# Kernel optimization log

Measured on AMD Instinct MI355X. Metric: run time of the kernel, lower is better.

The kernel has to match this reference:

```python
import jax, jax.numpy as jnp
import numpy as np

NUM_GRAPHS = 256
NUM_LAYERS = 4
HIDDEN = 256
N_FEATS = 9
VOCAB = 119
BN_EPS = 1e-5


def setup_inputs() -> dict:
    key = jax.random.key(0)
    ks = jax.random.split(key, 16)
    N, E, H = 10000, 320000, HIDDEN
    x = jax.random.randint(ks[0], (N, N_FEATS), 0, 2, dtype=jnp.int64)
    edge_index = jax.random.randint(ks[1], (2, E), 0, N, dtype=jnp.int64)
    batch_ids = jnp.sort(jax.random.randint(ks[2], (N,), 0, NUM_GRAPHS, dtype=jnp.int64))
    s = 1.0 / np.sqrt(H)
    emb = jax.random.normal(ks[3], (N_FEATS, VOCAB, H), jnp.float32) * 0.02
    W = jax.random.normal(ks[4], (NUM_LAYERS, H, H), jnp.float32) * s
    b = jnp.zeros((NUM_LAYERS, H), jnp.float32)
    gamma = jnp.ones((NUM_LAYERS, H), jnp.float32)
    beta = jnp.zeros((NUM_LAYERS, H), jnp.float32)
    mlp_W1 = jax.random.normal(ks[5], (H, H // 2), jnp.float32) * s
    mlp_b1 = jnp.zeros((H // 2,), jnp.float32)
    mlp_W2 = jax.random.normal(ks[6], (H // 2, H // 4), jnp.float32) * (1.0 / np.sqrt(H // 2))
    mlp_b2 = jnp.zeros((H // 4,), jnp.float32)
    mlp_W3 = jax.random.normal(ks[7], (H // 4, 1), jnp.float32) * (1.0 / np.sqrt(H // 4))
    mlp_b3 = jnp.zeros((1,), jnp.float32)
    return dict(x=x, edge_index=edge_index, batch_ids=batch_ids, emb=emb, W=W, b=b,
                gamma=gamma, beta=beta, mlp_W1=mlp_W1, mlp_b1=mlp_b1,
                mlp_W2=mlp_W2, mlp_b2=mlp_b2, mlp_W3=mlp_W3, mlp_b3=mlp_b3)


def reference(x, edge_index, batch_ids, emb, W, b, gamma, beta,
              mlp_W1, mlp_b1, mlp_W2, mlp_b2, mlp_W3, mlp_b3):
    N = x.shape[0]
    src, dst = edge_index[0], edge_index[1]

    # AtomEncoder: sum of per-feature embeddings. emb[f, x[:,f]] -> [N, 9, H]
    h = jnp.sum(emb[jnp.arange(N_FEATS), x], axis=1)

    # GCN normalization with self-loops: deg_i = 1 + in-degree, norm = deg^-1/2
    deg = 1.0 + jax.ops.segment_sum(jnp.ones_like(dst, jnp.float32), dst, num_segments=N)
    nrm = jax.lax.rsqrt(deg)
    edge_w = (nrm[src] * nrm[dst])[:, None]   # [E,1]
    self_w = (nrm * nrm)[:, None]             # [N,1]

    for l in range(NUM_LAYERS):
        identity = h
        hw = h @ W[l]                                     # dense GEMM [N,H]x[H,H]
        agg = jax.ops.segment_sum(hw[src] * edge_w, dst, num_segments=N) + hw * self_w
        h = agg + b[l]
        # BatchNorm1d (training statistics over nodes)
        mu = jnp.mean(h, axis=0)
        var = jnp.var(h, axis=0)
        h = (h - mu) * jax.lax.rsqrt(var + BN_EPS) * gamma[l] + beta[l]
        h = jax.nn.relu(h)
        h = h + identity  # residual

    # global mean pool over graph ids
    sums = jax.ops.segment_sum(h, batch_ids, num_segments=NUM_GRAPHS)
    cnt = jax.ops.segment_sum(jnp.ones((N,), jnp.float32), batch_ids, num_segments=NUM_GRAPHS)
    g = sums / jnp.maximum(cnt, 1.0)[:, None]             # [G, H]

    # MLP head [H, H/2, H/4, 1]
    g = jax.nn.relu(g @ mlp_W1 + mlp_b1)
    g = jax.nn.relu(g @ mlp_W2 + mlp_b2)
    return g @ mlp_W3 + mlp_b3
```

## Files before the change

### kernel.cpp

```cpp
#include <hip/hip_runtime.h>

#define HID 256
#define NFEAT 9
#define VOCAB 119
#define NLAYERS 4
#define NGRAPHS 256
#define BN_EPS 1e-5f

typedef short short8 __attribute__((ext_vector_type(8)));
typedef float floatx4 __attribute__((ext_vector_type(4)));

__device__ inline unsigned short f2bf(float f) {
    unsigned int u = __float_as_uint(f);
    unsigned int r = u + 0x7FFF + ((u >> 16) & 1);
    return (unsigned short)(r >> 16);
}
__device__ inline float bf2f(unsigned short u) {
    return __uint_as_float(((unsigned int)u) << 16);
}

__global__ __launch_bounds__(256) void setup_misc(
        const int* __restrict__ x, const float* __restrict__ emb,
        const float* __restrict__ W,
        int* __restrict__ degi, int* __restrict__ fillc, float* __restrict__ bnsums,
        unsigned short* __restrict__ wt, unsigned short* __restrict__ hbA,
        int N, int zb) {
    const int bx = blockIdx.x;
    const int tid = threadIdx.x;
    __shared__ float sw[32][33];
    __shared__ int xf[NFEAT];

    if (bx < zb) {
        int i = bx * 256 + tid;
        if (i < N) { degi[i] = 0; fillc[i] = 0; }
        if (bx == 0) {
            for (int j = tid; j < NLAYERS * 2 * HID; j += 256) bnsums[j] = 0.f;
        }
    } else if (bx < zb + 256) {
        int j = bx - zb;
        int l = j >> 6;
        int rem = j & 63;
        int k0 = (rem >> 3) * 32, n0 = (rem & 7) * 32;
        int c = tid & 31, r8 = tid >> 5;
        const float* Wl = W + (size_t)l * HID * HID;
        unsigned short* Wtl = wt + (size_t)l * HID * HID;
#pragma unroll
        for (int p = 0; p < 4; ++p) {
            int r = r8 + p * 8;
            sw[r][c] = Wl[(k0 + r) * HID + n0 + c];
        }
        __syncthreads();
#pragma unroll
        for (int p = 0; p < 4; ++p) {
            int r = r8 + p * 8;
            Wtl[(size_t)(n0 + r) * HID + k0 + c] = f2bf(sw[c][r]);
        }
    } else {
        int n = bx - zb - 256;
        if (n < N) {
            if (tid < NFEAT) xf[tid] = x[n * NFEAT + tid];
            __syncthreads();
            float s = 0.f;
#pragma unroll
            for (int f = 0; f < NFEAT; ++f) s += emb[(size_t)(f * VOCAB + xf[f]) * HID + tid];
            hbA[(size_t)n * HID + tid] = f2bf(s);
        }
    }
}

__global__ void deg_kernel(const int* __restrict__ dst, int* __restrict__ degi, int E) {
    int i = blockIdx.x * blockDim.x + threadIdx.x;
    if (i < E) atomicAdd(&degi[dst[i]], 1);
}

__global__ __launch_bounds__(1024) void scan_kernel(const int* __restrict__ degi,
                                                    int* __restrict__ row_ptr,
                                                    float* __restrict__ nrm, int N) {
    int tid = threadIdx.x;
    int ch = (N + 1023) >> 10;
    int i0 = tid * ch;
    int i1 = min(i0 + ch, N);
    if (i0 > N) i0 = N;
    int local = 0;
    for (int i = i0; i < i1; ++i) local += degi[i];
    int lane = tid & 63, wid = tid >> 6;
    int v = local;
#pragma unroll
    for (int off = 1; off < 64; off <<= 1) {
        int u = __shfl_up(v, off);
        if (lane >= off) v += u;
    }
    __shared__ int wsum[16];
    if (lane == 63) wsum[wid] = v;
    __syncthreads();
    if (tid < 16) {
        int w = wsum[tid];
#pragma unroll
        for (int off = 1; off < 16; off <<= 1) {
            int u = __shfl_up(w, off);
            if (tid >= off) w += u;
        }
        wsum[tid] = w;
    }
    __syncthreads();
    int base = (wid > 0 ? wsum[wid - 1] : 0) + (v - local);
    int run = base;
    for (int i = i0; i < i1; ++i) {
        int d = degi[i];
        row_ptr[i] = run;
        run += d;
        nrm[i] = rsqrtf(1.0f + (float)d);
    }
    if (tid == 0) row_ptr[N] = wsum[15];
}

__global__ void fill_kernel(const int* __restrict__ src, const int* __restrict__ dst,
                            const int* __restrict__ row_ptr, int* __restrict__ fill,
                            const float* __restrict__ nrm,
                            int2* __restrict__ edges, int E) {
    int i = blockIdx.x * blockDim.x + threadIdx.x;
    if (i < E) {
        int d = dst[i];
        int s = src[i];
        int pos = row_ptr[d] + atomicAdd(&fill[d], 1);
        int2 rec;
        rec.x = s;
        rec.y = __float_as_int(nrm[s] * nrm[d]);
        edges[pos] = rec;
    }
}

__global__ __launch_bounds__(256) void agg_shfl_kernel(const unsigned short* __restrict__ hb,
                                                       const int* __restrict__ row_ptr,
                                                       const int2* __restrict__ edges,
                                                       const float* __restrict__ nrm,
                                                       unsigned short* __restrict__ aggb, int N) {
    int tid = threadIdx.x;
    int wave = tid >> 6;
    int lane = tid & 63;
    int sub = lane >> 5;
    int sl = lane & 31;
    int n = blockIdx.x * 4 + wave;
    if (n >= N) return;
    int co = sl * 8;
    int s = row_ptr[n], e = row_ptr[n + 1];
    int len = e - s;
    int h0 = (len + 1) >> 1;
    int base = s + sub * h0;
    int cnt = sub ? (len - h0) : h0;
    float a[8];
#pragma unroll
    for (int j = 0; j < 8; ++j) a[j] = 0.f;

    int done = 0;
    while (done < cnt) {
        int m = min(32, cnt - done);
        int li = done + (sl < m ? sl : m - 1);
        int2 rec = edges[base + li];
        int j = 0;
        for (; j + 1 < m; j += 2) {
            int s0 = __shfl(rec.x, j, 32);
            int s1 = __shfl(rec.x, j + 1, 32);
            float w0 = __int_as_float(__shfl(rec.y, j, 32));
            float w1 = __int_as_float(__shfl(rec.y, j + 1, 32));
            short8 u0 = *(const short8*)&hb[(size_t)s0 * HID + co];
            short8 u1 = *(const short8*)&hb[(size_t)s1 * HID + co];
#pragma unroll
            for (int k = 0; k < 8; ++k)
                a[k] += w0 * bf2f((unsigned short)u0[k]) + w1 * bf2f((unsigned short)u1[k]);
        }
        if (j < m) {
            int s0 = __shfl(rec.x, j, 32);
            float w0 = __int_as_float(__shfl(rec.y, j, 32));
            short8 u0 = *(const short8*)&hb[(size_t)s0 * HID + co];
#pragma unroll
            for (int k = 0; k < 8; ++k) a[k] += w0 * bf2f((unsigned short)u0[k]);
        }
        done += m;
    }
#pragma unroll
    for (int j = 0; j < 8; ++j) a[j] += __shfl_xor(a[j], 32);
    if (sub == 0) {
        float nd = nrm[n];
        float sw2 = nd * nd;
        short8 us = *(const short8*)&hb[(size_t)n * HID + co];
        short8 o;
#pragma unroll
        for (int j = 0; j < 8; ++j) {
            float v = a[j] + sw2 * bf2f((unsigned short)us[j]);
            o[j] = (short)f2bf(v);
        }
        *(short8*)&aggb[(size_t)n * HID + co] = o;
    }
}

__global__ __launch_bounds__(256) void mfma_gemm128(const unsigned short* __restrict__ A,
                                                    const unsigned short* __restrict__ Bt,
                                                    const float* __restrict__ bias,
                                                    unsigned short* __restrict__ C,
                                                    float* __restrict__ sums, int M) {
    __shared__ unsigned short As[128][40];
    __shared__ unsigned short Bs[64][40];
    __shared__ float lsum[64];
    __shared__ float lsq[64];
    int tid = threadIdx.x;
    int row0 = blockIdx.x * 128;
    int col0 = blockIdx.y * 64;
    int lane = tid & 63;
    int wid = tid >> 6;
    int arow = tid >> 1;
    int akc = (tid & 1) * 16;
    int brow = tid >> 2;
    int bkc = (tid & 3) * 8;
    int wm = (wid & 1) * 64;
    int wn = (wid >> 1) * 32;
    int quad = lane >> 4;
    int ln = lane & 15;

    floatx4 acc[4][2];
#pragma unroll
    for (int r = 0; r < 4; ++r)
#pragma unroll
        for (int c = 0; c < 2; ++c) acc[r][c] = (floatx4){0.f, 0.f, 0.f, 0.f};

    if (tid < 64) { lsum[tid] = 0.f; lsq[tid] = 0.f; }

    for (int kk = 0; kk < HID; kk += 32) {
        short8 av0 = {0, 0, 0, 0, 0, 0, 0, 0};
        short8 av1 = {0, 0, 0, 0, 0, 0, 0, 0};
        int ar = row0 + arow;
        if (ar < M) {
            av0 = *(const short8*)&A[(size_t)ar * HID + kk + akc];
            av1 = *(const short8*)&A[(size_t)ar * HID + kk + akc + 8];
        }
        short8 bv = *(const short8*)&Bt[(size_t)(col0 + brow) * HID + kk + bkc];
        *(short8*)&As[arow][akc] = av0;
        *(short8*)&As[arow][akc + 8] = av1;
        *(short8*)&Bs[brow][bkc] = bv;
        __syncthreads();
        short8 bf0 = *(const short8*)&Bs[wn + ln][quad * 8];
        short8 bf1 = *(const short8*)&Bs[wn + 16 + ln][quad * 8];
#pragma unroll
        for (int r = 0; r < 4; ++r) {
            short8 af = *(const short8*)&As[wm + r * 16 + ln][quad * 8];
            acc[r][0] = __builtin_amdgcn_mfma_f32_16x16x32_bf16(af, bf0, acc[r][0], 0, 0, 0);
            acc[r][1] = __builtin_amdgcn_mfma_f32_16x16x32_bf16(af, bf1, acc[r][1], 0, 0, 0);
        }
        __syncthreads();
    }
    float bias0 = bias[col0 + wn + ln];
    float bias1 = bias[col0 + wn + 16 + ln];
    float p0 = 0.f, q0 = 0.f, p1 = 0.f, q1 = 0.f;
#pragma unroll
    for (int r = 0; r < 4; ++r) {
#pragma unroll
        for (int rr = 0; rr < 4; ++rr) {
            int row = row0 + wm + r * 16 + quad * 4 + rr;
            if (row < M) {
                float v0 = acc[r][0][rr] + bias0;
                float v1 = acc[r][1][rr] + bias1;
                C[(size_t)row * HID + col0 + wn + ln] = f2bf(v0);
                C[(size_t)row * HID + col0 + wn + 16 + ln] = f2bf(v1);
                p0 += v0; q0 += v0 * v0;
                p1 += v1; q1 += v1 * v1;
            }
        }
    }
    atomicAdd(&lsum[wn + ln], p0);
    atomicAdd(&lsq[wn + ln], q0);
    atomicAdd(&lsum[wn + 16 + ln], p1);
    atomicAdd(&lsq[wn + 16 + ln], q1);
    __syncthreads();
    if (tid < 64) {
        unsafeAtomicAdd(&sums[col0 + tid], lsum[tid]);
        unsafeAtomicAdd(&sums[HID + col0 + tid], lsq[tid]);
    }
}

__global__ __launch_bounds__(256) void bn_kernel(const unsigned short* __restrict__ hwb,
                                                 const float* __restrict__ sums,
                                                 const float* __restrict__ gamma,
                                                 const float* __restrict__ beta,
                                                 const unsigned short* __restrict__ hold,
                                                 unsigned short* __restrict__ hbnew, int N) {
    int i4 = blockIdx.x * blockDim.x + threadIdx.x;
    int base = i4 * 4;
    if (base >= N * HID) return;
    int c = base & (HID - 1);
    float invN = 1.0f / (float)N;
    float4 s4 = *(const float4*)&sums[c];
    float4 q4 = *(const float4*)&sums[HID + c];
    float4 g4 = *(const float4*)&gamma[c];
    float4 be4 = *(const float4*)&beta[c];
    ushort4 v = *(const ushort4*)&hwb[base];
    ushort4 r = *(const ushort4*)&hold[base];
    ushort4 o;
    {
        float mu = s4.x * invN, var = q4.x * invN - mu * mu;
        o.x = f2bf(fmaxf((bf2f(v.x) - mu) * g4.x * rsqrtf(var + BN_EPS) + be4.x, 0.f) + bf2f(r.x));
        mu = s4.y * invN; var = q4.y * invN - mu * mu;
        o.y = f2bf(fmaxf((bf2f(v.y) - mu) * g4.y * rsqrtf(var + BN_EPS) + be4.y, 0.f) + bf2f(r.y));
        mu = s4.z * invN; var = q4.z * invN - mu * mu;
        o.z = f2bf(fmaxf((bf2f(v.z) - mu) * g4.z * rsqrtf(var + BN_EPS) + be4.z, 0.f) + bf2f(r.z));
        mu = s4.w * invN; var = q4.w * invN - mu * mu;
        o.w = f2bf(fmaxf((bf2f(v.w) - mu) * g4.w * rsqrtf(var + BN_EPS) + be4.w, 0.f) + bf2f(r.w));
    }
    *(ushort4*)&hbnew[base] = o;
}

__device__ inline int lower_bound_g(const int* __restrict__ a, int n, int key) {
    int lo = 0, hi = n;
    while (lo < hi) {
        int mid = (lo + hi) >> 1;
        if (a[mid] < key) lo = mid + 1; else hi = mid;
    }
    return lo;
}

__global__ __launch_bounds__(256) void pool_mlp_bn_kernel(
        const unsigned short* __restrict__ hwb,
        const float* __restrict__ sums,
        const float* __restrict__ gamma,
        const float* __restrict__ beta,
        const unsigned short* __restrict__ resid,
        const int* __restrict__ batch, int N,
        const float* __restrict__ W1, const float* __restrict__ b1,
        const float* __restrict__ W2, const float* __restrict__ b2,
        const float* __restrict__ W3, const float* __restrict__ b3,
        float* __restrict__ out) {
    int g = blockIdx.x, tid = threadIdx.x;
    int lo = lower_bound_g(batch, N, g);
    int hi = lower_bound_g(batch, N, g + 1);
    float invN = 1.0f / (float)N;
    float mu = sums[tid] * invN;
    float var = sums[HID + tid] * invN - mu * mu;
    float sc = gamma[tid] * rsqrtf(var + BN_EPS);
    float be = beta[tid];
    float s = 0.f;
    for (int i = lo; i < hi; ++i) {
        float v = (bf2f(hwb[(size_t)i * HID + tid]) - mu) * sc + be;
        v = fmaxf(v, 0.f) + bf2f(resid[(size_t)i * HID + tid]);
        s += v;
    }
    __shared__ float gs[256];
    __shared__ float t1[128];
    __shared__ float t2[64];
    float inv = 1.0f / fmaxf((float)(hi - lo), 1.0f);
    gs[tid] = s * inv;
    __syncthreads();
    if (tid < 128) {
        float a = b1[tid];
        for (int k = 0; k < 256; ++k) a += gs[k] * W1[k * 128 + tid];
        t1[tid] = fmaxf(a, 0.f);
    }
    __syncthreads();
    if (tid < 64) {
        float a = b2[tid];
        for (int k = 0; k < 128; ++k) a += t1[k] * W2[k * 64 + tid];
        t2[tid] = fmaxf(a, 0.f);
    }
    __syncthreads();
    if (tid < 64) {
        float p = t2[tid] * W3[tid];
#pragma unroll
        for (int off = 32; off >= 1; off >>= 1) p += __shfl_down(p, off);
        if (tid == 0) out[g] = p + b3[0];
    }
}

extern "C" void kernel_launch(void* const* d_in, const int* in_sizes, int n_in,
                              void* d_out, int out_size, void* d_ws, size_t ws_size,
                              hipStream_t stream) {
    const int* x      = (const int*)d_in[0];
    const int* ei     = (const int*)d_in[1];
    const int* batch  = (const int*)d_in[2];
    const float* emb  = (const float*)d_in[3];
    const float* W    = (const float*)d_in[4];
    const float* b    = (const float*)d_in[5];
    const float* gamma= (const float*)d_in[6];
    const float* beta = (const float*)d_in[7];
    const float* W1   = (const float*)d_in[8];
    const float* b1   = (const float*)d_in[9];
    const float* W2   = (const float*)d_in[10];
    const float* b2   = (const float*)d_in[11];
    const float* W3   = (const float*)d_in[12];
    const float* b3   = (const float*)d_in[13];
    float* out = (float*)d_out;

    int N = in_sizes[0] / NFEAT;
    int E = in_sizes[1] / 2;
    const int* srcp = ei;
    const int* dstp = ei + E;

    char* ws = (char*)d_ws;
    auto alloc = [&](size_t bytes) -> char* {
        char* p = ws;
        ws += (bytes + 255) & ~(size_t)255;
        return p;
    };
    int* degi     = (int*)alloc((size_t)N * 4);
    int* row_ptr  = (int*)alloc((size_t)(N + 1) * 4);
    int* fillc    = (int*)alloc((size_t)N * 4);
    float* nrm    = (float*)alloc((size_t)N * 4);
    int2* edges   = (int2*)alloc((size_t)E * 8);
    unsigned short* hbA  = (unsigned short*)alloc((size_t)N * HID * 2);
    unsigned short* hbB  = (unsigned short*)alloc((size_t)N * HID * 2);
    unsigned short* aggb = (unsigned short*)alloc((size_t)N * HID * 2);
    unsigned short* hwb  = (unsigned short*)alloc((size_t)N * HID * 2);
    unsigned short* wt   = (unsigned short*)alloc((size_t)NLAYERS * HID * HID * 2);
    float* bnsums = (float*)alloc((size_t)NLAYERS * 2 * HID * 4);

    int zb = (N + 255) / 256;
    int miscGrid = zb + 256 + N;
    setup_misc<<<miscGrid, 256, 0, stream>>>(x, emb, W, degi, fillc, bnsums, wt, hbA, N, zb);
    deg_kernel<<<(E + 255) / 256, 256, 0, stream>>>(dstp, degi, E);
    scan_kernel<<<1, 1024, 0, stream>>>(degi, row_ptr, nrm, N);
    fill_kernel<<<(E + 255) / 256, 256, 0, stream>>>(srcp, dstp, row_ptr, fillc, nrm, edges, E);

    unsigned short* hbcur = hbA;
    unsigned short* hboth = hbB;
    for (int l = 0; l < NLAYERS; ++l) {
        float* lsums = bnsums + (size_t)l * 2 * HID;
        agg_shfl_kernel<<<(N + 3) / 4, 256, 0, stream>>>(hbcur, row_ptr, edges, nrm, aggb, N);
        dim3 ggrid((N + 127) / 128, 4);
        mfma_gemm128<<<ggrid, 256, 0, stream>>>(aggb, wt + (size_t)l * HID * HID,
                                                b + (size_t)l * HID, hwb, lsums, N);
        if (l < NLAYERS - 1) {
            bn_kernel<<<((size_t)N * HID / 4 + 255) / 256, 256, 0, stream>>>(
                hwb, lsums, gamma + (size_t)l * HID, beta + (size_t)l * HID,
                hbcur, hboth, N);
            unsigned short* tb = hbcur; hbcur = hboth; hboth = tb;
        }
    }

    pool_mlp_bn_kernel<<<NGRAPHS, 256, 0, stream>>>(
        hwb, bnsums + (size_t)3 * 2 * HID, gamma + (size_t)3 * HID, beta + (size_t)3 * HID,
        hbcur, batch, N, W1, b1, W2, b2, W3, b3, out);
}
```

Baseline: 302.4 us.

## Split aggregation into column halves with four edge groups per wave

The aggregation kernel now launches twice as many blocks, each handling half of the 256 feature columns. Each wave is split into four 16-lane groups that process different edges at the same time, instead of two 32-lane halves covering all columns. This raises memory-level parallelism per wave and shortens the serial edge loop per node, which should help hide gather latency. In exchange, edge records are read twice (once per column half) and the reduction needs an extra cross-lane shuffle step.

```diff
diff --git a/kernel.cpp b/kernel.cpp
--- a/kernel.cpp
+++ b/kernel.cpp
@@ -130,65 +130,69 @@
     }
 }
 
-__global__ __launch_bounds__(256) void agg_shfl_kernel(const unsigned short* __restrict__ hb,
-                                                       const int* __restrict__ row_ptr,
-                                                       const int2* __restrict__ edges,
-                                                       const float* __restrict__ nrm,
-                                                       unsigned short* __restrict__ aggb, int N) {
+__global__ __launch_bounds__(256) void agg_g4_kernel(const unsigned short* __restrict__ hb,
+                                                     const int* __restrict__ row_ptr,
+                                                     const int2* __restrict__ edges,
+                                                     const float* __restrict__ nrm,
+                                                     unsigned short* __restrict__ aggb, int N) {
+    int bx = blockIdx.x;
+    int half = bx & 1;
     int tid = threadIdx.x;
     int wave = tid >> 6;
     int lane = tid & 63;
-    int sub = lane >> 5;
-    int sl = lane & 31;
-    int n = blockIdx.x * 4 + wave;
+    int g = lane >> 4;
+    int sl = lane & 15;
+    int n = (bx >> 1) * 4 + wave;
     if (n >= N) return;
-    int co = sl * 8;
+    int co = half * 128 + sl * 8;
+    const unsigned short* hbc = hb + co;
     int s = row_ptr[n], e = row_ptr[n + 1];
     int len = e - s;
-    int h0 = (len + 1) >> 1;
-    int base = s + sub * h0;
-    int cnt = sub ? (len - h0) : h0;
     float a[8];
 #pragma unroll
-    for (int j = 0; j < 8; ++j) a[j] = 0.f;
+    for (int k = 0; k < 8; ++k) a[k] = 0.f;
 
     int done = 0;
-    while (done < cnt) {
-        int m = min(32, cnt - done);
-        int li = done + (sl < m ? sl : m - 1);
-        int2 rec = edges[base + li];
+    while (done < len) {
+        int m = min(64, len - done);
+        int li = done + (lane < m ? lane : m - 1);
+        int2 rec = edges[s + li];
+        int mq = m & ~3;
         int j = 0;
-        for (; j + 1 < m; j += 2) {
-            int s0 = __shfl(rec.x, j, 32);
-            int s1 = __shfl(rec.x, j + 1, 32);
-            float w0 = __int_as_float(__shfl(rec.y, j, 32));
-            float w1 = __int_as_float(__shfl(rec.y, j + 1, 32));
-            short8 u0 = *(const short8*)&hb[(size_t)s0 * HID + co];
-            short8 u1 = *(const short8*)&hb[(size_t)s1 * HID + co];
-#pragma unroll
-            for (int k = 0; k < 8; ++k)
-                a[k] += w0 * bf2f((unsigned short)u0[k]) + w1 * bf2f((unsigned short)u1[k]);
+        for (; j < mq; j += 4) {
+            int jj = j + g;
+            int src = __shfl(rec.x, jj, 64);
+            float w = __int_as_float(__shfl(rec.y, jj, 64));
+            short8 u = *(const short8*)&hbc[(size_t)src * HID];
+#pragma unroll
+            for (int k = 0; k < 8; ++k) a[k] += w * bf2f((unsigned short)u[k]);
         }
         if (j < m) {
-            int s0 = __shfl(rec.x, j, 32);
-            float w0 = __int_as_float(__shfl(rec.y, j, 32));
-            short8 u0 = *(const short8*)&hb[(size_t)s0 * HID + co];
-#pragma unroll
-            for (int k = 0; k < 8; ++k) a[k] += w0 * bf2f((unsigned short)u0[k]);
+            int jj = j + g;
+            int cj = jj < m ? jj : (m - 1);
+            int src = __shfl(rec.x, cj, 64);
+            float w = __int_as_float(__shfl(rec.y, cj, 64));
+            if (jj >= m) w = 0.f;
+            short8 u = *(const short8*)&hbc[(size_t)src * HID];
+#pragma unroll
+            for (int k = 0; k < 8; ++k) a[k] += w * bf2f((unsigned short)u[k]);
         }
         done += m;
     }
 #pragma unroll
-    for (int j = 0; j < 8; ++j) a[j] += __shfl_xor(a[j], 32);
-    if (sub == 0) {
+    for (int k = 0; k < 8; ++k) {
+        a[k] += __shfl_xor(a[k], 16);
+        a[k] += __shfl_xor(a[k], 32);
+    }
+    if (g == 0) {
         float nd = nrm[n];
         float sw2 = nd * nd;
-        short8 us = *(const short8*)&hb[(size_t)n * HID + co];
+        short8 us = *(const short8*)&hbc[(size_t)n * HID];
         short8 o;
 #pragma unroll
-        for (int j = 0; j < 8; ++j) {
-            float v = a[j] + sw2 * bf2f((unsigned short)us[j]);
-            o[j] = (short)f2bf(v);
+        for (int k = 0; k < 8; ++k) {
+            float v = a[k] + sw2 * bf2f((unsigned short)us[k]);
+            o[k] = (short)f2bf(v);
         }
         *(short8*)&aggb[(size_t)n * HID + co] = o;
     }
@@ -419,9 +423,10 @@
 
     unsigned short* hbcur = hbA;
     unsigned short* hboth = hbB;
+    int aggGrid = ((N + 3) / 4) * 2;
     for (int l = 0; l < NLAYERS; ++l) {
         float* lsums = bnsums + (size_t)l * 2 * HID;
-        agg_shfl_kernel<<<(N + 3) / 4, 256, 0, stream>>>(hbcur, row_ptr, edges, nrm, aggb, N);
+        agg_g4_kernel<<<aggGrid, 256, 0, stream>>>(hbcur, row_ptr, edges, nrm, aggb, N);
         dim3 ggrid((N + 127) / 128, 4);
         mfma_gemm128<<<ggrid, 256, 0, stream>>>(aggb, wt + (size_t)l * HID * HID,
                                                 b + (size_t)l * HID, hwb, lsums, N);
```

Measured after the change: 301.8 us. No clear change (-0.2%).
